# Performance work log

Measured on AMD Instinct MI355X. Metric: run time of the kernel, lower is better.

Reference implementation:

```python
import jax, jax.numpy as jnp
import numpy as np

N, E, HID, HEADS, EDIM = 32768, 262144, 64, 4, 3
C = HID  # per-head out channels (concat=False -> mean over heads)


def setup_inputs() -> dict:
    key = jax.random.key(0)
    ks = jax.random.split(key, 24)
    g = lambda k, shape, s=1.0: jax.random.normal(k, shape, jnp.float32) * s
    s_lin = 1.0 / np.sqrt(HID)
    s_edge = 1.0 / np.sqrt(EDIM)
    s_att = 1.0 / np.sqrt(C)
    inp = {
        "t": jnp.zeros((1,), jnp.float32),
        "h": g(ks[0], (N, HID)),
        "edge_index": jax.random.randint(ks[1], (2, E), 0, N, jnp.int32),
        "edge_attr": g(ks[2], (E, EDIM)),
        "W1": g(ks[3], (HID, HEADS * C), s_lin),
        "We1": g(ks[4], (EDIM, HEADS * C), s_edge),
        "att_src1": g(ks[5], (HEADS, C), s_att),
        "att_dst1": g(ks[6], (HEADS, C), s_att),
        "att_edge1": g(ks[7], (HEADS, C), s_att),
        "b1": jnp.zeros((C,), jnp.float32),
        "ln_g1": jnp.ones((HID,), jnp.float32),
        "ln_b1": jnp.zeros((HID,), jnp.float32),
        # last GAT layer's lin weight is scaled by 0.1 in __init__
        "W2": g(ks[8], (HID, HEADS * C), s_lin) * 0.1,
        "We2": g(ks[9], (EDIM, HEADS * C), s_edge),
        "att_src2": g(ks[10], (HEADS, C), s_att),
        "att_dst2": g(ks[11], (HEADS, C), s_att),
        "att_edge2": g(ks[12], (HEADS, C), s_att),
        "b2": jnp.zeros((C,), jnp.float32),
        "ln_g2": jnp.ones((HID,), jnp.float32),
        "ln_b2": jnp.zeros((HID,), jnp.float32),
    }
    return inp


def _gat_layer(z, src, dst, edge_attr, W, We, a_src, a_dst, a_edge, b):
    # PyG GATConv(edge_dim>0, concat=False, add_self_loops=False), eval mode (no dropout)
    x = (z @ W).reshape(-1, HEADS, C)                      # [N,H,C]
    alpha_s = jnp.einsum("nhc,hc->nh", x, a_src)           # [N,H]
    alpha_d = jnp.einsum("nhc,hc->nh", x, a_dst)           # [N,H]
    e = (edge_attr @ We).reshape(-1, HEADS, C)             # [E,H,C]
    alpha_e = jnp.einsum("ehc,hc->eh", e, a_edge)          # [E,H]
    logit = jax.nn.leaky_relu(alpha_s[src] + alpha_d[dst] + alpha_e, 0.2)  # [E,H]
    # segment softmax over incoming edges of each destination node
    m = jax.lax.stop_gradient(jax.ops.segment_max(logit, dst, num_segments=N))
    ex = jnp.exp(logit - m[dst])
    denom = jax.ops.segment_sum(ex, dst, num_segments=N)
    alpha = ex / (denom[dst] + 1e-16)                      # [E,H]
    msg = x[src] * alpha[..., None]                        # [E,H,C] gather + weight
    out = jax.ops.segment_sum(msg, dst, num_segments=N)    # [N,H,C] scatter-add
    return out.mean(axis=1) + b                            # head mean + bias -> [N,C]


def _layernorm(x, g, b, eps=1e-5):
    mu = x.mean(-1, keepdims=True)
    var = ((x - mu) ** 2).mean(-1, keepdims=True)
    return (x - mu) * jax.lax.rsqrt(var + eps) * g + b


def reference(t, h, edge_index, edge_attr, W1, We1, att_src1, att_dst1, att_edge1, b1,
              ln_g1, ln_b1, W2, We2, att_src2, att_dst2, att_edge2, b2, ln_g2, ln_b2):
    del t  # autonomous ODE func: t unused
    src, dst = edge_index[0], edge_index[1]
    z = h
    z = jax.nn.silu(_layernorm(_gat_layer(z, src, dst, edge_attr, W1, We1, att_src1, att_dst1, att_edge1, b1), ln_g1, ln_b1))
    z = jax.nn.silu(_layernorm(_gat_layer(z, src, dst, edge_attr, W2, We2, att_src2, att_dst2, att_edge2, b2), ln_g2, ln_b2))
    return z
```

## Files before the change

kernel.cpp:

```cpp
#include <hip/hip_runtime.h>
#include <math.h>

#define HIDDEN 64
#define HEADS 4
#define HC 256
#define CAP 64

typedef __attribute__((ext_vector_type(8))) short short8;
typedef __attribute__((ext_vector_type(4))) float f32x4;

__device__ __forceinline__ unsigned short f2bf(float f) {
    unsigned int u = __float_as_uint(f);
    u += 0x7fffu + ((u >> 16) & 1u);
    return (unsigned short)(u >> 16);
}

__device__ __forceinline__ unsigned short f2h(float f) {
    _Float16 h = (_Float16)f;
    return *(unsigned short*)&h;
}

__device__ __forceinline__ float h2f(unsigned int u) {
    unsigned short s = (unsigned short)u;
    _Float16 h = *(_Float16*)&s;
    return (float)h;
}

__global__ __launch_bounds__(256) void k_fused(const int* __restrict__ dst,
                                               const int* __restrict__ src,
                                               const float* __restrict__ ea,
                                               const float* __restrict__ h,
                                               const float* __restrict__ W1f,
                                               const float* __restrict__ W2f,
                                               const float* __restrict__ We1,
                                               const float* __restrict__ at1,
                                               const float* __restrict__ We2,
                                               const float* __restrict__ at2,
                                               int* __restrict__ counts,
                                               uint2* __restrict__ eb,
                                               ushort* __restrict__ zb,
                                               ushort* __restrict__ wt1,
                                               ushort* __restrict__ wt2,
                                               float* __restrict__ wr, int E) {
    int t = threadIdx.x, b = blockIdx.x;
    if (b < 1024) {
        int e = b * 256 + t;
        if (e < E) {
            int d = dst[e];
            int c = atomicAdd(&counts[d], 1);
            if (c < CAP) {
                size_t slot = (size_t)d * CAP + c;
                unsigned int lo = (unsigned int)(src[e] & 0xffff)
                                | ((unsigned int)f2h(ea[e * 3 + 0]) << 16);
                unsigned int hi = (unsigned int)f2h(ea[e * 3 + 1])
                                | ((unsigned int)f2h(ea[e * 3 + 2]) << 16);
                eb[slot] = make_uint2(lo, hi);
            }
        }
    } else if (b < 3072) {
        int i = (b - 1024) * 256 + t;
        float4 v = ((const float4*)h)[i];
        ushort4 o;
        o.x = f2bf(v.x); o.y = f2bf(v.y); o.z = f2bf(v.z); o.w = f2bf(v.w);
        ((ushort4*)zb)[i] = o;
    } else if (b < 3136) {
        int j = (b - 3072) * 256 + t;
        int c = j >> 6, k = j & 63;
        wt1[j] = f2bf(W1f[k * HC + c]);
        wt2[j] = f2bf(W2f[k * HC + c]);
    } else {
        int wv = t >> 6, lane = t & 63;
#pragma unroll
        for (int it = 0; it < 6; ++it) {
            int comb = wv + it * 4;
            int layer = comb / 12;
            int dh = comb % 12;
            int d = dh >> 2, hh = dh & 3;
            const float* We = layer ? We2 : We1;
            const float* at = layer ? at2 : at1;
            float v = We[d * HC + hh * HIDDEN + lane] * at[hh * HIDDEN + lane];
            for (int o = 32; o > 0; o >>= 1) v += __shfl_down(v, o);
            if (lane == 0) wr[layer * 16 + d * HEADS + hh] = v;
        }
    }
}

__global__ __launch_bounds__(256) void k_tmfma(const ushort* __restrict__ zb,
                                               const ushort* __restrict__ wt,
                                               const float* __restrict__ asw,
                                               const float* __restrict__ adw,
                                               ushort* __restrict__ xb,
                                               float* __restrict__ as_,
                                               float* __restrict__ ad_) {
    int wave = threadIdx.x >> 6, lane = threadIdx.x & 63;
    int q = lane & 15, quad = lane >> 4;
    int row0 = blockIdx.x * 64 + wave * 16;

    const ushort* zrow = zb + (size_t)(row0 + q) * 64 + quad * 8;
    short8 a0 = *(const short8*)(zrow);
    short8 a1 = *(const short8*)(zrow + 32);

#pragma unroll
    for (int h = 0; h < 4; ++h) {
        float vs[4] = {0.f, 0.f, 0.f, 0.f};
        float vd[4] = {0.f, 0.f, 0.f, 0.f};
#pragma unroll
        for (int nt = 0; nt < 4; ++nt) {
            int col0 = h * 64 + nt * 16;
            const ushort* wrow = wt + (size_t)(col0 + q) * 64 + quad * 8;
            short8 b0 = *(const short8*)(wrow);
            short8 b1 = *(const short8*)(wrow + 32);
            f32x4 acc = {0.f, 0.f, 0.f, 0.f};
            acc = __builtin_amdgcn_mfma_f32_16x16x32_bf16(a0, b0, acc, 0, 0, 0);
            acc = __builtin_amdgcn_mfma_f32_16x16x32_bf16(a1, b1, acc, 0, 0, 0);
            int c = col0 + q;
            float aw = asw[c], dw = adw[c];
#pragma unroll
            for (int r = 0; r < 4; ++r) {
                float v = acc[r];
                xb[(size_t)(row0 + quad * 4 + r) * HC + c] = f2bf(v);
                vs[r] += v * aw;
                vd[r] += v * dw;
            }
        }
#pragma unroll
        for (int o = 1; o < 16; o <<= 1) {
#pragma unroll
            for (int r = 0; r < 4; ++r) {
                vs[r] += __shfl_xor(vs[r], o);
                vd[r] += __shfl_xor(vd[r], o);
            }
        }
        if (q < 4) {
            int n = row0 + quad * 4 + q;
            as_[n * 4 + h] = vs[q];
            ad_[n * 4 + h] = vd[q];
        }
    }
}

__global__ __launch_bounds__(256) void k_aggregate(
        const ushort* __restrict__ xb, const uint2* __restrict__ eb,
        const int* __restrict__ counts,
        const float* __restrict__ as_, const float* __restrict__ ad_,
        const float* __restrict__ wrl,
        const float* __restrict__ bias, const float* __restrict__ lng,
        const float* __restrict__ lnb, float* __restrict__ outf,
        ushort* __restrict__ outb, int N) {
    int lane = threadIdx.x & 63;
    int h = lane >> 4, sub = lane & 15;
    int e = sub & 1, g = sub >> 1;
    int wid = blockIdx.x * 4 + (threadIdx.x >> 6);
    int nwaves = gridDim.x * 4;

    float w0 = wrl[h], w1 = wrl[4 + h], w2 = wrl[8 + h];

    float bs[8], gm[8], bt[8];
#pragma unroll
    for (int k = 0; k < 8; ++k) {
        bs[k] = bias[g * 8 + k];
        gm[k] = lng[g * 8 + k];
        bt[k] = lnb[g * 8 + k];
    }

    for (int n = wid; n < N; n += nwaves) {
        int deg = counts[n];
        if (deg > CAP) deg = CAP;
        size_t base = (size_t)n * CAP;
        float ad4 = ad_[n * 4 + h];

        float ssum = 0.f;
        float acc[8];
#pragma unroll
        for (int k = 0; k < 8; ++k) acc[k] = 0.f;

        for (int cs = 0; cs < deg; cs += 16) {
            int idx = cs + sub;
            int s_sub = 0;
            float wgt = 0.f;
            if (idx < deg) {
                uint2 rec = eb[base + idx];
                s_sub = (int)(rec.x & 0xffffu);
                float lg = as_[s_sub * 4 + h] + ad4
                         + h2f(rec.x >> 16) * w0
                         + h2f(rec.y) * w1
                         + h2f(rec.y >> 16) * w2;
                lg = (lg >= 0.f) ? lg : 0.2f * lg;
                wgt = __expf(lg);
            }
            ssum += wgt;

            int jb = deg - cs; if (jb > 16) jb = 16;
            for (int j4 = 0; j4 < jb; j4 += 4) {
                int sl0 = h * 16 + j4 + e;
                int sl1 = h * 16 + j4 + 2 + e;
                float q0 = __shfl(wgt, sl0);
                int s0 = __shfl(s_sub, sl0);
                float q1 = __shfl(wgt, sl1);
                int s1 = __shfl(s_sub, sl1);
                uint4 r0 = *(const uint4*)&xb[(size_t)s0 * HC + h * HIDDEN + g * 8];
                uint4 r1 = *(const uint4*)&xb[(size_t)s1 * HC + h * HIDDEN + g * 8];
                unsigned int u0[4] = {r0.x, r0.y, r0.z, r0.w};
                unsigned int u1[4] = {r1.x, r1.y, r1.z, r1.w};
#pragma unroll
                for (int k = 0; k < 4; ++k) {
                    acc[2 * k + 0] += q0 * __uint_as_float(u0[k] << 16);
                    acc[2 * k + 1] += q0 * __uint_as_float(u0[k] & 0xffff0000u);
                    acc[2 * k + 0] += q1 * __uint_as_float(u1[k] << 16);
                    acc[2 * k + 1] += q1 * __uint_as_float(u1[k] & 0xffff0000u);
                }
            }
        }
#pragma unroll
        for (int o = 1; o < 16; o <<= 1) ssum += __shfl_xor(ssum, o);
        float winv = 1.f / (ssum + 1e-16f);
#pragma unroll
        for (int k = 0; k < 8; ++k) acc[k] *= winv;
#pragma unroll
        for (int k = 0; k < 8; ++k) {
            acc[k] += __shfl_xor(acc[k], 1);
            acc[k] += __shfl_xor(acc[k], 16);
            acc[k] += __shfl_xor(acc[k], 32);
        }

        float u8[8], s1 = 0.f;
#pragma unroll
        for (int k = 0; k < 8; ++k) {
            u8[k] = acc[k] * 0.25f + bs[k];
            s1 += u8[k];
        }
#pragma unroll
        for (int o = 2; o < 16; o <<= 1) s1 += __shfl_xor(s1, o);
        float mu = s1 * (1.f / 64.f);
        float s2 = 0.f;
#pragma unroll
        for (int k = 0; k < 8; ++k) {
            float d = u8[k] - mu;
            s2 += d * d;
        }
#pragma unroll
        for (int o = 2; o < 16; o <<= 1) s2 += __shfl_xor(s2, o);
        float rstd = rsqrtf(s2 * (1.f / 64.f) + 1e-5f);
        float r[8];
#pragma unroll
        for (int k = 0; k < 8; ++k) {
            float y = (u8[k] - mu) * rstd * gm[k] + bt[k];
            r[k] = y / (1.f + __expf(-y));
        }
        if ((lane & 49) == 0) {
            if (outb) {
                uint4 pk;
                pk.x = (unsigned)f2bf(r[0]) | ((unsigned)f2bf(r[1]) << 16);
                pk.y = (unsigned)f2bf(r[2]) | ((unsigned)f2bf(r[3]) << 16);
                pk.z = (unsigned)f2bf(r[4]) | ((unsigned)f2bf(r[5]) << 16);
                pk.w = (unsigned)f2bf(r[6]) | ((unsigned)f2bf(r[7]) << 16);
                *(uint4*)&outb[(size_t)n * HIDDEN + g * 8] = pk;
            } else {
                float4* o4 = (float4*)&outf[(size_t)n * HIDDEN + g * 8];
                o4[0] = make_float4(r[0], r[1], r[2], r[3]);
                o4[1] = make_float4(r[4], r[5], r[6], r[7]);
            }
        }
    }
}


extern "C" void kernel_launch(void* const* d_in, const int* in_sizes, int n_in,
                              void* d_out, int out_size, void* d_ws, size_t ws_size,
                              hipStream_t stream) {
    const float* h   = (const float*)d_in[1];
    const int*   ei  = (const int*)d_in[2];
    const float* ea  = (const float*)d_in[3];
    const float* W1  = (const float*)d_in[4];
    const float* We1 = (const float*)d_in[5];
    const float* as1 = (const float*)d_in[6];
    const float* ad1 = (const float*)d_in[7];
    const float* ae1 = (const float*)d_in[8];
    const float* b1  = (const float*)d_in[9];
    const float* lg1 = (const float*)d_in[10];
    const float* lb1 = (const float*)d_in[11];
    const float* W2  = (const float*)d_in[12];
    const float* We2 = (const float*)d_in[13];
    const float* as2 = (const float*)d_in[14];
    const float* ad2 = (const float*)d_in[15];
    const float* ae2 = (const float*)d_in[16];
    const float* b2  = (const float*)d_in[17];
    const float* lg2 = (const float*)d_in[18];
    const float* lb2 = (const float*)d_in[19];

    const int N = in_sizes[1] / HIDDEN;
    const int E = in_sizes[2] / 2;
    const int* srcp = ei;
    const int* dstp = ei + E;

    char* w = (char*)d_ws;
    ushort* xb    = (ushort*)w; w += (size_t)N * HC * 2;
    ushort* zb    = (ushort*)w; w += (size_t)N * HIDDEN * 2;
    float* as_    = (float*)w;  w += (size_t)N * HEADS * 4;
    float* adv    = (float*)w;  w += (size_t)N * HEADS * 4;
    ushort* wt1   = (ushort*)w; w += 16384 * 2;
    ushort* wt2   = (ushort*)w; w += 16384 * 2;
    float* wr     = (float*)w;  w += 128;
    int* counts   = (int*)w;    w += (size_t)N * 4;
    uint2* eb     = (uint2*)w;  w += (size_t)N * CAP * 8;

    hipMemsetAsync(counts, 0, (size_t)N * 4, stream);
    k_fused<<<3137, 256, 0, stream>>>(dstp, srcp, ea, h, W1, W2,
                                      We1, ae1, We2, ae2,
                                      counts, eb, zb, wt1, wt2, wr, E);

    k_tmfma<<<N / 64, 256, 0, stream>>>(zb, wt1, as1, ad1, xb, as_, adv);
    k_aggregate<<<4096, 256, 0, stream>>>(xb, eb, counts, as_, adv, wr,
                                          b1, lg1, lb1, nullptr, zb, N);
    k_tmfma<<<N / 64, 256, 0, stream>>>(zb, wt2, as2, ad2, xb, as_, adv);
    k_aggregate<<<4096, 256, 0, stream>>>(xb, eb, counts, as_, adv, wr + 16,
                                          b2, lg2, lb2, (float*)d_out, nullptr, N);
}
```

Before: 217.8 us.

## Reorder GAT to aggregate raw features before projection via matrix associativity

Instead of projecting every node to 4 heads x 64 channels and gathering that 256-wide bf16 row per edge, the aggregation now gathers the 64-wide input row and produces per-head weighted sums, and the projection with a head-stacked, head-mean-prescaled weight runs afterwards as a K=256 MFMA GEMM fused with bias, LayerNorm and SiLU. The attention score vectors are folded into W (W·a) so alpha_src/dst become 64-wide dot products, computed in a small kernel for layer 1 and fused into the output kernel for layer 2. This cuts the per-edge gather traffic by about four times, at the cost of an extra N x 256 intermediate write/read and more cross-lane shuffles in the aggregation loop.

```diff
diff --git a/kernel.cpp b/kernel.cpp
--- a/kernel.cpp
+++ b/kernel.cpp
@@ -25,6 +25,9 @@
     _Float16 h = *(_Float16*)&s;
     return (float)h;
 }
+
+__device__ __forceinline__ float bflo(unsigned int u) { return __uint_as_float(u << 16); }
+__device__ __forceinline__ float bfhi(unsigned int u) { return __uint_as_float(u & 0xffff0000u); }
 
 __global__ __launch_bounds__(256) void k_fused(const int* __restrict__ dst,
                                                const int* __restrict__ src,
@@ -33,14 +36,19 @@
                                                const float* __restrict__ W1f,
                                                const float* __restrict__ W2f,
                                                const float* __restrict__ We1,
-                                               const float* __restrict__ at1,
+                                               const float* __restrict__ ae1,
                                                const float* __restrict__ We2,
-                                               const float* __restrict__ at2,
+                                               const float* __restrict__ ae2,
+                                               const float* __restrict__ ats1,
+                                               const float* __restrict__ atd1,
+                                               const float* __restrict__ ats2,
+                                               const float* __restrict__ atd2,
                                                int* __restrict__ counts,
                                                uint2* __restrict__ eb,
                                                ushort* __restrict__ zb,
-                                               ushort* __restrict__ wt1,
-                                               ushort* __restrict__ wt2,
+                                               ushort* __restrict__ wst1,
+                                               ushort* __restrict__ wst2,
+                                               float* __restrict__ wsv,
                                                float* __restrict__ wr, int E) {
     int t = threadIdx.x, b = blockIdx.x;
     if (b < 1024) {
@@ -63,11 +71,29 @@
         ushort4 o;
         o.x = f2bf(v.x); o.y = f2bf(v.y); o.z = f2bf(v.z); o.w = f2bf(v.w);
         ((ushort4*)zb)[i] = o;
-    } else if (b < 3136) {
+    } else if (b < 3200) {
         int j = (b - 3072) * 256 + t;
-        int c = j >> 6, k = j & 63;
-        wt1[j] = f2bf(W1f[k * HC + c]);
-        wt2[j] = f2bf(W2f[k * HC + c]);
+        const float* W = (j < 16384) ? W1f : W2f;
+        ushort* wst = (j < 16384) ? wst1 : wst2;
+        int i = j & 16383;
+        int c = i >> 8, k = i & 255;
+        wst[i] = f2bf(0.25f * W[(k & 63) * HC + (k >> 6) * 64 + c]);
+    } else if (b < 3204) {
+        int r = b - 3200;
+        const float* W = (r >> 1) ? W2f : W1f;
+        const float* at;
+        if (r == 0) at = ats1; else if (r == 1) at = atd1;
+        else if (r == 2) at = ats2; else at = atd2;
+        int hh = t >> 6, k = t & 63;
+        const float4* wrow = (const float4*)&W[k * HC + hh * 64];
+        const float4* arow = (const float4*)&at[hh * 64];
+        float v = 0.f;
+#pragma unroll
+        for (int c4 = 0; c4 < 16; ++c4) {
+            float4 wv = wrow[c4], av = arow[c4];
+            v += wv.x * av.x + wv.y * av.y + wv.z * av.z + wv.w * av.w;
+        }
+        wsv[r * 256 + hh * 64 + k] = v;
     } else {
         int wv = t >> 6, lane = t & 63;
 #pragma unroll
@@ -77,7 +103,7 @@
             int dh = comb % 12;
             int d = dh >> 2, hh = dh & 3;
             const float* We = layer ? We2 : We1;
-            const float* at = layer ? at2 : at1;
+            const float* at = layer ? ae2 : ae1;
             float v = We[d * HC + hh * HIDDEN + lane] * at[hh * HIDDEN + lane];
             for (int o = 32; o > 0; o >>= 1) v += __shfl_down(v, o);
             if (lane == 0) wr[layer * 16 + d * HEADS + hh] = v;
@@ -85,94 +111,57 @@
     }
 }
 
-__global__ __launch_bounds__(256) void k_tmfma(const ushort* __restrict__ zb,
-                                               const ushort* __restrict__ wt,
-                                               const float* __restrict__ asw,
-                                               const float* __restrict__ adw,
-                                               ushort* __restrict__ xb,
+__global__ __launch_bounds__(256) void k_alpha(const ushort* __restrict__ zb,
+                                               const float* __restrict__ wsv,
                                                float* __restrict__ as_,
                                                float* __restrict__ ad_) {
-    int wave = threadIdx.x >> 6, lane = threadIdx.x & 63;
-    int q = lane & 15, quad = lane >> 4;
-    int row0 = blockIdx.x * 64 + wave * 16;
-
-    const ushort* zrow = zb + (size_t)(row0 + q) * 64 + quad * 8;
-    short8 a0 = *(const short8*)(zrow);
-    short8 a1 = *(const short8*)(zrow + 32);
-
-#pragma unroll
-    for (int h = 0; h < 4; ++h) {
-        float vs[4] = {0.f, 0.f, 0.f, 0.f};
-        float vd[4] = {0.f, 0.f, 0.f, 0.f};
-#pragma unroll
-        for (int nt = 0; nt < 4; ++nt) {
-            int col0 = h * 64 + nt * 16;
-            const ushort* wrow = wt + (size_t)(col0 + q) * 64 + quad * 8;
-            short8 b0 = *(const short8*)(wrow);
-            short8 b1 = *(const short8*)(wrow + 32);
-            f32x4 acc = {0.f, 0.f, 0.f, 0.f};
-            acc = __builtin_amdgcn_mfma_f32_16x16x32_bf16(a0, b0, acc, 0, 0, 0);
-            acc = __builtin_amdgcn_mfma_f32_16x16x32_bf16(a1, b1, acc, 0, 0, 0);
-            int c = col0 + q;
-            float aw = asw[c], dw = adw[c];
-#pragma unroll
-            for (int r = 0; r < 4; ++r) {
-                float v = acc[r];
-                xb[(size_t)(row0 + quad * 4 + r) * HC + c] = f2bf(v);
-                vs[r] += v * aw;
-                vd[r] += v * dw;
-            }
-        }
-#pragma unroll
-        for (int o = 1; o < 16; o <<= 1) {
-#pragma unroll
-            for (int r = 0; r < 4; ++r) {
-                vs[r] += __shfl_xor(vs[r], o);
-                vd[r] += __shfl_xor(vd[r], o);
-            }
-        }
-        if (q < 4) {
-            int n = row0 + quad * 4 + q;
-            as_[n * 4 + h] = vs[q];
-            ad_[n * 4 + h] = vd[q];
-        }
-    }
+    __shared__ float ls[512];
+    int t = threadIdx.x;
+    ls[t] = wsv[t];
+    ls[t + 256] = wsv[t + 256];
+    __syncthreads();
+    int n = blockIdx.x * 256 + t;
+    const ushort* zr = zb + (size_t)n * HIDDEN;
+    float as[4] = {0.f, 0.f, 0.f, 0.f};
+    float ad[4] = {0.f, 0.f, 0.f, 0.f};
+#pragma unroll
+    for (int ks = 0; ks < 8; ++ks) {
+        uint4 v = *(const uint4*)(zr + ks * 8);
+        unsigned int uu[4] = {v.x, v.y, v.z, v.w};
+#pragma unroll
+        for (int p = 0; p < 4; ++p) {
+            float f0 = bflo(uu[p]), f1 = bfhi(uu[p]);
+            int k = ks * 8 + p * 2;
+#pragma unroll
+            for (int hh = 0; hh < 4; ++hh) {
+                as[hh] += f0 * ls[hh * 64 + k] + f1 * ls[hh * 64 + k + 1];
+                ad[hh] += f0 * ls[256 + hh * 64 + k] + f1 * ls[256 + hh * 64 + k + 1];
+            }
+        }
+    }
+    *(float4*)&as_[n * 4] = make_float4(as[0], as[1], as[2], as[3]);
+    *(float4*)&ad_[n * 4] = make_float4(ad[0], ad[1], ad[2], ad[3]);
 }
 
 __global__ __launch_bounds__(256) void k_aggregate(
-        const ushort* __restrict__ xb, const uint2* __restrict__ eb,
+        const ushort* __restrict__ zb, const uint2* __restrict__ eb,
         const int* __restrict__ counts,
         const float* __restrict__ as_, const float* __restrict__ ad_,
         const float* __restrict__ wrl,
-        const float* __restrict__ bias, const float* __restrict__ lng,
-        const float* __restrict__ lnb, float* __restrict__ outf,
-        ushort* __restrict__ outb, int N) {
+        ushort* __restrict__ agg, int N) {
     int lane = threadIdx.x & 63;
     int h = lane >> 4, sub = lane & 15;
-    int e = sub & 1, g = sub >> 1;
     int wid = blockIdx.x * 4 + (threadIdx.x >> 6);
     int nwaves = gridDim.x * 4;
-
     float w0 = wrl[h], w1 = wrl[4 + h], w2 = wrl[8 + h];
-
-    float bs[8], gm[8], bt[8];
-#pragma unroll
-    for (int k = 0; k < 8; ++k) {
-        bs[k] = bias[g * 8 + k];
-        gm[k] = lng[g * 8 + k];
-        bt[k] = lnb[g * 8 + k];
-    }
 
     for (int n = wid; n < N; n += nwaves) {
         int deg = counts[n];
         if (deg > CAP) deg = CAP;
         size_t base = (size_t)n * CAP;
         float ad4 = ad_[n * 4 + h];
-
         float ssum = 0.f;
-        float acc[8];
-#pragma unroll
-        for (int k = 0; k < 8; ++k) acc[k] = 0.f;
+        float acc0 = 0.f, acc1 = 0.f, acc2 = 0.f, acc3 = 0.f;
 
         for (int cs = 0; cs < deg; cs += 16) {
             int idx = cs + sub;
@@ -191,76 +180,146 @@
             ssum += wgt;
 
             int jb = deg - cs; if (jb > 16) jb = 16;
-            for (int j4 = 0; j4 < jb; j4 += 4) {
-                int sl0 = h * 16 + j4 + e;
-                int sl1 = h * 16 + j4 + 2 + e;
-                float q0 = __shfl(wgt, sl0);
-                int s0 = __shfl(s_sub, sl0);
-                float q1 = __shfl(wgt, sl1);
-                int s1 = __shfl(s_sub, sl1);
-                uint4 r0 = *(const uint4*)&xb[(size_t)s0 * HC + h * HIDDEN + g * 8];
-                uint4 r1 = *(const uint4*)&xb[(size_t)s1 * HC + h * HIDDEN + g * 8];
-                unsigned int u0[4] = {r0.x, r0.y, r0.z, r0.w};
-                unsigned int u1[4] = {r1.x, r1.y, r1.z, r1.w};
-#pragma unroll
-                for (int k = 0; k < 4; ++k) {
-                    acc[2 * k + 0] += q0 * __uint_as_float(u0[k] << 16);
-                    acc[2 * k + 1] += q0 * __uint_as_float(u0[k] & 0xffff0000u);
-                    acc[2 * k + 0] += q1 * __uint_as_float(u1[k] << 16);
-                    acc[2 * k + 1] += q1 * __uint_as_float(u1[k] & 0xffff0000u);
+            for (int j = 0; j < jb; j += 4) {
+                int s_g = __shfl(s_sub, j + h);
+                uint2 zv = *(const uint2*)&zb[(size_t)s_g * HIDDEN + sub * 4];
+#pragma unroll
+                for (int e = 0; e < 4; ++e) {
+                    float we = __shfl(wgt, h * 16 + j + e);
+                    unsigned int zx = (unsigned int)__shfl((int)zv.x, e * 16 + sub);
+                    unsigned int zy = (unsigned int)__shfl((int)zv.y, e * 16 + sub);
+                    acc0 += we * bflo(zx);
+                    acc1 += we * bfhi(zx);
+                    acc2 += we * bflo(zy);
+                    acc3 += we * bfhi(zy);
                 }
             }
         }
 #pragma unroll
         for (int o = 1; o < 16; o <<= 1) ssum += __shfl_xor(ssum, o);
         float winv = 1.f / (ssum + 1e-16f);
-#pragma unroll
-        for (int k = 0; k < 8; ++k) acc[k] *= winv;
-#pragma unroll
-        for (int k = 0; k < 8; ++k) {
-            acc[k] += __shfl_xor(acc[k], 1);
-            acc[k] += __shfl_xor(acc[k], 16);
-            acc[k] += __shfl_xor(acc[k], 32);
-        }
-
-        float u8[8], s1 = 0.f;
-#pragma unroll
-        for (int k = 0; k < 8; ++k) {
-            u8[k] = acc[k] * 0.25f + bs[k];
-            s1 += u8[k];
-        }
-#pragma unroll
-        for (int o = 2; o < 16; o <<= 1) s1 += __shfl_xor(s1, o);
-        float mu = s1 * (1.f / 64.f);
-        float s2 = 0.f;
-#pragma unroll
-        for (int k = 0; k < 8; ++k) {
-            float d = u8[k] - mu;
-            s2 += d * d;
-        }
-#pragma unroll
-        for (int o = 2; o < 16; o <<= 1) s2 += __shfl_xor(s2, o);
-        float rstd = rsqrtf(s2 * (1.f / 64.f) + 1e-5f);
-        float r[8];
-#pragma unroll
-        for (int k = 0; k < 8; ++k) {
-            float y = (u8[k] - mu) * rstd * gm[k] + bt[k];
-            r[k] = y / (1.f + __expf(-y));
-        }
-        if ((lane & 49) == 0) {
-            if (outb) {
-                uint4 pk;
-                pk.x = (unsigned)f2bf(r[0]) | ((unsigned)f2bf(r[1]) << 16);
-                pk.y = (unsigned)f2bf(r[2]) | ((unsigned)f2bf(r[3]) << 16);
-                pk.z = (unsigned)f2bf(r[4]) | ((unsigned)f2bf(r[5]) << 16);
-                pk.w = (unsigned)f2bf(r[6]) | ((unsigned)f2bf(r[7]) << 16);
-                *(uint4*)&outb[(size_t)n * HIDDEN + g * 8] = pk;
-            } else {
-                float4* o4 = (float4*)&outf[(size_t)n * HIDDEN + g * 8];
-                o4[0] = make_float4(r[0], r[1], r[2], r[3]);
-                o4[1] = make_float4(r[4], r[5], r[6], r[7]);
-            }
-        }
+        uint2 o2;
+        o2.x = (unsigned)f2bf(acc0 * winv) | ((unsigned)f2bf(acc1 * winv) << 16);
+        o2.y = (unsigned)f2bf(acc2 * winv) | ((unsigned)f2bf(acc3 * winv) << 16);
+        *(uint2*)&agg[(size_t)n * HC + h * 64 + sub * 4] = o2;
+    }
+}
+
+__global__ __launch_bounds__(256) void k_out(const ushort* __restrict__ agg,
+                                             const ushort* __restrict__ wst,
+                                             const float* __restrict__ bias,
+                                             const float* __restrict__ lng,
+                                             const float* __restrict__ lnb,
+                                             const float* __restrict__ wsv2,
+                                             float* __restrict__ as_,
+                                             float* __restrict__ ad_,
+                                             float* __restrict__ outf,
+                                             ushort* __restrict__ outb) {
+    int lane = threadIdx.x & 63;
+    int q = lane & 15, quad = lane >> 4;
+    int row0 = blockIdx.x * 64 + (threadIdx.x >> 6) * 16;
+
+    const ushort* arow = agg + (size_t)(row0 + q) * HC + quad * 8;
+    short8 a[8];
+#pragma unroll
+    for (int ks = 0; ks < 8; ++ks) a[ks] = *(const short8*)(arow + ks * 32);
+
+    f32x4 acc[4];
+#pragma unroll
+    for (int nt = 0; nt < 4; ++nt) {
+        const ushort* brow = wst + (size_t)(nt * 16 + q) * HC + quad * 8;
+        f32x4 c4 = {0.f, 0.f, 0.f, 0.f};
+#pragma unroll
+        for (int ks = 0; ks < 8; ++ks) {
+            short8 bfr = *(const short8*)(brow + ks * 32);
+            c4 = __builtin_amdgcn_mfma_f32_16x16x32_bf16(a[ks], bfr, c4, 0, 0, 0);
+        }
+        acc[nt] = c4;
+    }
+
+    float u[4][4], s1[4] = {0.f, 0.f, 0.f, 0.f};
+#pragma unroll
+    for (int nt = 0; nt < 4; ++nt) {
+        float bv = bias[nt * 16 + q];
+#pragma unroll
+        for (int r = 0; r < 4; ++r) { u[nt][r] = acc[nt][r] + bv; s1[r] += u[nt][r]; }
+    }
+#pragma unroll
+    for (int o = 1; o < 16; o <<= 1)
+#pragma unroll
+        for (int r = 0; r < 4; ++r) s1[r] += __shfl_xor(s1[r], o);
+    float mu[4], s2[4] = {0.f, 0.f, 0.f, 0.f};
+#pragma unroll
+    for (int r = 0; r < 4; ++r) mu[r] = s1[r] * (1.f / 64.f);
+#pragma unroll
+    for (int nt = 0; nt < 4; ++nt)
+#pragma unroll
+        for (int r = 0; r < 4; ++r) { float d = u[nt][r] - mu[r]; s2[r] += d * d; }
+#pragma unroll
+    for (int o = 1; o < 16; o <<= 1)
+#pragma unroll
+        for (int r = 0; r < 4; ++r) s2[r] += __shfl_xor(s2[r], o);
+    float rstd[4];
+#pragma unroll
+    for (int r = 0; r < 4; ++r) rstd[r] = rsqrtf(s2[r] * (1.f / 64.f) + 1e-5f);
+
+    float rv[4][4];
+#pragma unroll
+    for (int nt = 0; nt < 4; ++nt) {
+        float gv = lng[nt * 16 + q], bb = lnb[nt * 16 + q];
+#pragma unroll
+        for (int r = 0; r < 4; ++r) {
+            float y = (u[nt][r] - mu[r]) * rstd[r] * gv + bb;
+            rv[nt][r] = y / (1.f + __expf(-y));
+        }
+    }
+
+    if (outb) {
+#pragma unroll
+        for (int nt = 0; nt < 4; ++nt)
+#pragma unroll
+            for (int r = 0; r < 4; ++r)
+                outb[(size_t)(row0 + quad * 4 + r) * HIDDEN + nt * 16 + q] = f2bf(rv[nt][r]);
+        float vs[4][4] = {{0.f}}, vd[4][4] = {{0.f}};
+#pragma unroll
+        for (int hh = 0; hh < 4; ++hh)
+#pragma unroll
+            for (int nt = 0; nt < 4; ++nt) {
+                float wsc = wsv2[hh * 64 + nt * 16 + q];
+                float wdc = wsv2[256 + hh * 64 + nt * 16 + q];
+#pragma unroll
+                for (int r = 0; r < 4; ++r) {
+                    vs[r][hh] += rv[nt][r] * wsc;
+                    vd[r][hh] += rv[nt][r] * wdc;
+                }
+            }
+#pragma unroll
+        for (int o = 1; o < 16; o <<= 1)
+#pragma unroll
+            for (int r = 0; r < 4; ++r)
+#pragma unroll
+                for (int hh = 0; hh < 4; ++hh) {
+                    vs[r][hh] += __shfl_xor(vs[r][hh], o);
+                    vd[r][hh] += __shfl_xor(vd[r][hh], o);
+                }
+        if (q < 4) {
+#pragma unroll
+            for (int r = 0; r < 4; ++r) {
+                float sv = (q == 0) ? vs[r][0] : (q == 1) ? vs[r][1]
+                         : (q == 2) ? vs[r][2] : vs[r][3];
+                float dv = (q == 0) ? vd[r][0] : (q == 1) ? vd[r][1]
+                         : (q == 2) ? vd[r][2] : vd[r][3];
+                int n = row0 + quad * 4 + r;
+                as_[n * 4 + q] = sv;
+                ad_[n * 4 + q] = dv;
+            }
+        }
+    } else {
+#pragma unroll
+        for (int nt = 0; nt < 4; ++nt)
+#pragma unroll
+            for (int r = 0; r < 4; ++r)
+                outf[(size_t)(row0 + quad * 4 + r) * HIDDEN + nt * 16 + q] = rv[nt][r];
     }
 }
 
@@ -294,25 +353,28 @@
     const int* dstp = ei + E;
 
     char* w = (char*)d_ws;
-    ushort* xb    = (ushort*)w; w += (size_t)N * HC * 2;
+    ushort* agg   = (ushort*)w; w += (size_t)N * HC * 2;
     ushort* zb    = (ushort*)w; w += (size_t)N * HIDDEN * 2;
     float* as_    = (float*)w;  w += (size_t)N * HEADS * 4;
     float* adv    = (float*)w;  w += (size_t)N * HEADS * 4;
-    ushort* wt1   = (ushort*)w; w += 16384 * 2;
-    ushort* wt2   = (ushort*)w; w += 16384 * 2;
+    ushort* wst1  = (ushort*)w; w += 16384 * 2;
+    ushort* wst2  = (ushort*)w; w += 16384 * 2;
+    float* wsv    = (float*)w;  w += 1024 * 4;
     float* wr     = (float*)w;  w += 128;
     int* counts   = (int*)w;    w += (size_t)N * 4;
     uint2* eb     = (uint2*)w;  w += (size_t)N * CAP * 8;
 
     hipMemsetAsync(counts, 0, (size_t)N * 4, stream);
-    k_fused<<<3137, 256, 0, stream>>>(dstp, srcp, ea, h, W1, W2,
+    k_fused<<<3205, 256, 0, stream>>>(dstp, srcp, ea, h, W1, W2,
                                       We1, ae1, We2, ae2,
-                                      counts, eb, zb, wt1, wt2, wr, E);
-
-    k_tmfma<<<N / 64, 256, 0, stream>>>(zb, wt1, as1, ad1, xb, as_, adv);
-    k_aggregate<<<4096, 256, 0, stream>>>(xb, eb, counts, as_, adv, wr,
-                                          b1, lg1, lb1, nullptr, zb, N);
-    k_tmfma<<<N / 64, 256, 0, stream>>>(zb, wt2, as2, ad2, xb, as_, adv);
-    k_aggregate<<<4096, 256, 0, stream>>>(xb, eb, counts, as_, adv, wr + 16,
-                                          b2, lg2, lb2, (float*)d_out, nullptr, N);
-}
+                                      as1, ad1, as2, ad2,
+                                      counts, eb, zb, wst1, wst2, wsv, wr, E);
+
+    k_alpha<<<N / 256, 256, 0, stream>>>(zb, wsv, as_, adv);
+    k_aggregate<<<4096, 256, 0, stream>>>(zb, eb, counts, as_, adv, wr, agg, N);
+    k_out<<<N / 64, 256, 0, stream>>>(agg, wst1, b1, lg1, lb1, wsv + 512,
+                                      as_, adv, nullptr, zb);
+    k_aggregate<<<4096, 256, 0, stream>>>(zb, eb, counts, as_, adv, wr + 16, agg, N);
+    k_out<<<N / 64, 256, 0, stream>>>(agg, wst2, b2, lg2, lb2, nullptr,
+                                      nullptr, nullptr, (float*)d_out, nullptr);
+}
```

New measurement: 194.0 us. 1.12x faster.
